# Performance work log

Hardware: AMD Instinct MI355X
Metric: run time of the kernel (lower is better)

Reference implementation:

```python
import jax, jax.numpy as jnp
import numpy as np

N_NODES = 100000
N_EDGES = 1600000
K = 3


def _cheb_conv(x, row, col, w, W, b):
    # SpMM: out[row] += w * x[col]
    def spmm(v):
        return jax.ops.segment_sum(w[:, None] * v[col], row, num_segments=N_NODES)
    Ts = [x, spmm(x)]
    for _ in range(2, K):
        Ts.append(2.0 * spmm(Ts[-1]) - Ts[-2])
    return jnp.concatenate(Ts, axis=-1) @ W.T + b


def setup_inputs() -> dict:
    key = jax.random.key(0)
    ks = jax.random.split(key, 12)
    inp = {
        "x": jax.random.normal(ks[0], (N_NODES, 128), dtype=jnp.float32),
        "edge_index": jax.random.randint(ks[1], (2, N_EDGES), 0, N_NODES, dtype=jnp.int32),
        "edge_weight": jax.random.normal(ks[2], (N_EDGES,), dtype=jnp.float32) * 0.05,
        "W_in": jax.random.normal(ks[3], (128, K * 128), dtype=jnp.float32) * (1.0 / np.sqrt(K * 128)),
        "b_in": jnp.zeros((128,), dtype=jnp.float32),
        "W_h1": jax.random.normal(ks[4], (128, K * 128), dtype=jnp.float32) * (1.0 / np.sqrt(K * 128)),
        "b_h1": jnp.zeros((128,), dtype=jnp.float32),
        "W_h2": jax.random.normal(ks[5], (128, K * 128), dtype=jnp.float32) * (1.0 / np.sqrt(K * 128)),
        "b_h2": jnp.zeros((128,), dtype=jnp.float32),
        "W_out": jax.random.normal(ks[6], (64, K * 128), dtype=jnp.float32) * (1.0 / np.sqrt(K * 128)),
        "b_out": jnp.zeros((64,), dtype=jnp.float32),
    }
    return inp


def reference(x, edge_index, edge_weight, W_in, b_in, W_h1, b_h1, W_h2, b_h2, W_out, b_out):
    row, col = edge_index[0], edge_index[1]
    # dropout is inactive at inference (training=False)
    h = jax.nn.relu(_cheb_conv(x, row, col, edge_weight, W_in, b_in))
    for (W, b) in ((W_h1, b_h1), (W_h2, b_h2)):
        h = jax.nn.relu(_cheb_conv(h, row, col, edge_weight, W, b) + h)  # residual
    out = _cheb_conv(h, row, col, edge_weight, W_out, b_out)
    return out
```

## Files before the change

### kernel.cpp

```cpp
#include <hip/hip_runtime.h>
#include <hip/hip_bf16.h>
#include <stdint.h>
#include <stddef.h>

#define N_NODES 100000
#define N_EDGES 1600000
#define FEAT 128
#define NB_SCAN ((N_NODES + 255) / 256)
#define LDS_PITCH 136
#define CAP 24
#define NL (CAP / 4)
#define NBKT ((N_NODES + 255) / 256)
#define BCAP 8160
#define EPB 2048

typedef __attribute__((ext_vector_type(8))) short bf16x8;
typedef __attribute__((ext_vector_type(4))) float f32x4;
typedef unsigned short u16;

__device__ __forceinline__ float bf2f(u16 u) {
    union { unsigned int i; float f; } v; v.i = ((unsigned int)u) << 16; return v.f;
}
__device__ __forceinline__ u16 f2bf(float f) {
    union { float f; unsigned int i; } v; v.f = f;
    unsigned int x = v.i;
    return (u16)((x + 0x7fffu + ((x >> 16) & 1u)) >> 16);
}


__global__ void hist_kernel(const int* __restrict__ rows, int* __restrict__ counts) {
    int e = blockIdx.x * blockDim.x + threadIdx.x;
    if (e < N_EDGES) {
        int r = rows[e];
        r = min(max(r, 0), N_NODES - 1);
        atomicAdd(&counts[r], 1);
    }
}

__global__ void reduce_counts_kernel(const int* __restrict__ counts, int* __restrict__ bsum) {
    __shared__ int s[256];
    int i = blockIdx.x * 256 + threadIdx.x;
    int v = (i < N_NODES) ? counts[i] : 0;
    s[threadIdx.x] = v; __syncthreads();
    for (int off = 128; off > 0; off >>= 1) {
        if (threadIdx.x < off) s[threadIdx.x] += s[threadIdx.x + off];
        __syncthreads();
    }
    if (threadIdx.x == 0) bsum[blockIdx.x] = s[0];
}

__global__ void scan_bsums_kernel(int* __restrict__ bsum, int* __restrict__ row_ptr) {
    __shared__ int s[512];
    int t = threadIdx.x;
    int v = (t < NB_SCAN) ? bsum[t] : 0;
    s[t] = v; __syncthreads();
    for (int off = 1; off < 512; off <<= 1) {
        int x = (t >= off) ? s[t - off] : 0;
        __syncthreads();
        s[t] += x;
        __syncthreads();
    }
    if (t < NB_SCAN) bsum[t] = s[t] - v;
    if (t == NB_SCAN - 1) row_ptr[N_NODES] = s[t];
}

__global__ void write_rowptr_kernel(int* __restrict__ counts, const int* __restrict__ bsum,
                                    int* __restrict__ row_ptr) {
    __shared__ int s[256];
    int i = blockIdx.x * 256 + threadIdx.x;
    int v = (i < N_NODES) ? counts[i] : 0;
    s[threadIdx.x] = v; __syncthreads();
    for (int off = 1; off < 256; off <<= 1) {
        int x = (threadIdx.x >= off) ? s[threadIdx.x - off] : 0;
        __syncthreads();
        s[threadIdx.x] += x;
        __syncthreads();
    }
    if (i < N_NODES) {
        row_ptr[i] = bsum[blockIdx.x] + s[threadIdx.x] - v;
        counts[i] = 0;
    }
}

__global__ void scatter_kernel(const int* __restrict__ rows, const int* __restrict__ cols,
                               const float* __restrict__ w, const int* __restrict__ row_ptr,
                               int* __restrict__ fill, int2* __restrict__ ecw) {
    int e = blockIdx.x * blockDim.x + threadIdx.x;
    if (e < N_EDGES) {
        int r = rows[e];
        r = min(max(r, 0), N_NODES - 1);
        int pos = row_ptr[r] + atomicAdd(&fill[r], 1);
        pos = min(max(pos, 0), N_EDGES - 1);
        int c = cols[e];
        c = min(max(c, 0), N_NODES - 1);
        ecw[pos] = make_int2(c, __float_as_int(w[e]));
    }
}


__global__ __launch_bounds__(256) void bucket_p1_kernel(const int* __restrict__ rows,
                                                        const int* __restrict__ cols,
                                                        const float* __restrict__ w,
                                                        int* __restrict__ gcnt,
                                                        int2* __restrict__ bbuf) {
    __shared__ int s_cnt[NBKT];
    __shared__ int s_base[NBKT];
    int tid = threadIdx.x;
    for (int b = tid; b < NBKT; b += 256) s_cnt[b] = 0;
    __syncthreads();
    int e0 = blockIdx.x * EPB;
#pragma unroll
    for (int it = 0; it < EPB / 256; ++it) {
        int e = e0 + it * 256 + tid;
        if (e < N_EDGES) {
            int r = min(max(rows[e], 0), N_NODES - 1);
            atomicAdd(&s_cnt[r >> 8], 1);
        }
    }
    __syncthreads();
    for (int b = tid; b < NBKT; b += 256) {
        s_base[b] = atomicAdd(&gcnt[b], s_cnt[b]);
        s_cnt[b] = 0;
    }
    __syncthreads();
#pragma unroll
    for (int it = 0; it < EPB / 256; ++it) {
        int e = e0 + it * 256 + tid;
        if (e < N_EDGES) {
            int r = min(max(rows[e], 0), N_NODES - 1);
            int b = r >> 8;
            int k = atomicAdd(&s_cnt[b], 1);
            int pos = min(s_base[b] + k, BCAP - 1);
            int c = min(max(cols[e], 0), N_NODES - 1);
            bbuf[(size_t)b * BCAP + pos] = make_int2(c | ((r & 255) << 20), __float_as_int(w[e]));
        }
    }
}

__global__ void scan_gcnt_kernel(const int* __restrict__ gcnt, int* __restrict__ bsum,
                                 int* __restrict__ row_ptr) {
    __shared__ int s[512];
    int t = threadIdx.x;
    int v = (t < NBKT) ? min(gcnt[t], BCAP) : 0;
    s[t] = v; __syncthreads();
    for (int off = 1; off < 512; off <<= 1) {
        int x = (t >= off) ? s[t - off] : 0;
        __syncthreads();
        s[t] += x;
        __syncthreads();
    }
    if (t < NBKT) bsum[t] = s[t] - v;
    if (t == NBKT - 1) row_ptr[N_NODES] = s[t];
}

__global__ __launch_bounds__(256) void bucket_finalize_kernel(const int* __restrict__ gcnt,
                                                              const int* __restrict__ bsum,
                                                              const int2* __restrict__ bbuf,
                                                              int* __restrict__ row_ptr,
                                                              int2* __restrict__ ecw) {
    __shared__ int s_cnt[256];
    __shared__ int s_pos[256];
    int b = blockIdx.x, tid = threadIdx.x;
    int base = bsum[b];
    int cnt = min(gcnt[b], BCAP);
    s_cnt[tid] = 0; __syncthreads();
    for (int i = tid; i < cnt; i += 256)
        atomicAdd(&s_cnt[bbuf[(size_t)b * BCAP + i].x >> 20], 1);
    __syncthreads();
    int v = s_cnt[tid];
    s_pos[tid] = v; __syncthreads();
    for (int off = 1; off < 256; off <<= 1) {
        int x = (tid >= off) ? s_pos[tid - off] : 0;
        __syncthreads();
        s_pos[tid] += x;
        __syncthreads();
    }
    int excl = s_pos[tid] - v;
    int r = b * 256 + tid;
    if (r < N_NODES) row_ptr[r] = base + excl;
    s_cnt[tid] = excl;
    __syncthreads();
    for (int i = tid; i < cnt; i += 256) {
        int2 p = bbuf[(size_t)b * BCAP + i];
        int rl = p.x >> 20;
        int pos = base + atomicAdd(&s_cnt[rl], 1);
        pos = min(max(pos, 0), N_EDGES - 1);
        ecw[pos] = make_int2(p.x & 0xFFFFF, p.y);
    }
}

__device__ __forceinline__ float w_fold(const float* W, int o, int k) {
    if (k < 128)      return W[o * 384 + k] - W[o * 384 + 256 + k];
    else if (k < 256) return W[o * 384 + k];
    else              return 2.0f * W[o * 384 + k];
}

__global__ void prep_w_kernel(const float* __restrict__ W, u16* __restrict__ Wp, int O) {
    int i = blockIdx.x * blockDim.x + threadIdx.x;
    if (i >= O * 384) return;
    int o = i / 384, k = i % 384;
    Wp[i] = f2bf(w_fold(W, o, k));
}

__global__ void prep_w2_all_kernel(const float* __restrict__ Wa, const float* __restrict__ Wb,
                                   const float* __restrict__ Wc, const float* __restrict__ Wd,
                                   u16* __restrict__ Pa, u16* __restrict__ Pb,
                                   u16* __restrict__ Pc, u16* __restrict__ Pd) {
    int i = blockIdx.x * blockDim.x + threadIdx.x;
    const float* W; u16* P; int il;
    if (i < 6144)       { W = Wa; P = Pa; il = i; }
    else if (i < 12288) { W = Wb; P = Pb; il = i - 6144; }
    else if (i < 18432) { W = Wc; P = Pc; il = i - 12288; }
    else if (i < 21504) { W = Wd; P = Pd; il = i - 18432; }
    else return;
    int ot = il / 768;
    int rem = il % 768;
    int kk = rem / 64;
    int l = rem % 64;
    int q = l >> 4, r = l & 15;
    int o = ot * 16 + r;
    int kbase = kk * 32 + q * 8;
#pragma unroll
    for (int j = 0; j < 8; ++j)
        P[(size_t)il * 8 + j] = f2bf(w_fold(W, o, kbase + j));
}


__global__ void cvt_kernel(const float* __restrict__ x, u16* __restrict__ y) {
    int i = blockIdx.x * blockDim.x + threadIdx.x;
    if (i >= N_NODES * FEAT / 4) return;
    float4 v = ((const float4*)x)[i];
    ushort4 o;
    o.x = f2bf(v.x); o.y = f2bf(v.y); o.z = f2bf(v.z); o.w = f2bf(v.w);
    ((ushort4*)y)[i] = o;
}


__device__ __forceinline__ void load_meta(const int2* __restrict__ ecw, int s, int n,
                                          int lane, int& call, float& wall) {
    int idx = s + max(0, min(lane, n - 1));
    idx = min(idx, N_EDGES - 1);
    int2 cw = ecw[idx];
    call = cw.x;
    wall = (lane < n) ? __int_as_float(cw.y) : 0.f;
}

__device__ __forceinline__ void issue_row(const u16* __restrict__ X, int call,
                                          int g, int f, bf16x8* q) {
#pragma unroll
    for (int k = 0; k < NL; ++k) {
        int col = __shfl(call, k * 4 + g);
        q[k] = *(const bf16x8*)(X + (size_t)col * FEAT + f * 8);
    }
}

__device__ __forceinline__ void reduce_row(const bf16x8* q, float wall,
                                           int g, float* acc) {
#pragma unroll
    for (int k = 0; k < NL; ++k) {
        float wj = __shfl(wall, k * 4 + g);
#pragma unroll
        for (int j = 0; j < 8; ++j) acc[j] += wj * bf2f((u16)q[k][j]);
    }
}


__global__ __launch_bounds__(256) void spmm1_kernel(const int* __restrict__ row_ptr,
                                                    const int2* __restrict__ ecw,
                                                    const u16* __restrict__ X,
                                                    u16* __restrict__ Y) {
    int lane = threadIdx.x & 63;
    int g = lane >> 4, f = lane & 15;
    int rr = (blockIdx.x * blockDim.x + threadIdx.x) >> 6;

    int s = row_ptr[rr], e = row_ptr[rr + 1];
    float acc[8];
#pragma unroll
    for (int j = 0; j < 8; ++j) acc[j] = 0.f;

    {
        int call; float wall;
        load_meta(ecw, s, min(e - s, CAP), lane, call, wall);
        bf16x8 q[NL];
        issue_row(X, call, g, f, q);
        reduce_row(q, wall, g, acc);
    }
    for (int cs = s + CAP; cs < e; cs += CAP) {
        int c2; float w2;
        load_meta(ecw, cs, min(e - cs, CAP), lane, c2, w2);
        bf16x8 qt[NL];
        issue_row(X, c2, g, f, qt);
        reduce_row(qt, w2, g, acc);
    }

#pragma unroll
    for (int j = 0; j < 8; ++j) {
        acc[j] += __shfl_xor(acc[j], 16);
        acc[j] += __shfl_xor(acc[j], 32);
    }
    if (g == 0) {
        u16 tmp[8];
#pragma unroll
        for (int j = 0; j < 8; ++j) tmp[j] = f2bf(acc[j]);
        *(bf16x8*)(Y + (size_t)rr * FEAT + f * 8) = *(const bf16x8*)tmp;
    }
}


__device__ __forceinline__ void gather4(const int* __restrict__ row_ptr,
                                        const int2* __restrict__ ecw,
                                        const u16* __restrict__ X,
                                        int r0, int lane, int g, int f,
                                        float acc[4][8]) {
    int s[4], e[4];
    int call[4]; float wall[4];
#pragma unroll
    for (int y = 0; y < 4; ++y) {
        s[y] = row_ptr[r0 + y];
        e[y] = row_ptr[r0 + y + 1];
    }
#pragma unroll
    for (int y = 0; y < 4; ++y)
        load_meta(ecw, s[y], min(e[y] - s[y], CAP), lane, call[y], wall[y]);
#pragma unroll
    for (int y = 0; y < 4; ++y)
#pragma unroll
        for (int j = 0; j < 8; ++j) acc[y][j] = 0.f;

    bf16x8 q0[NL], q1[NL], q2[NL], q3[NL];
    issue_row(X, call[0], g, f, q0);
    issue_row(X, call[1], g, f, q1);
    reduce_row(q0, wall[0], g, acc[0]);
    issue_row(X, call[2], g, f, q2);
    reduce_row(q1, wall[1], g, acc[1]);
    issue_row(X, call[3], g, f, q3);
    reduce_row(q2, wall[2], g, acc[2]);
    reduce_row(q3, wall[3], g, acc[3]);

#pragma unroll
    for (int y = 0; y < 4; ++y) {
        for (int cs = s[y] + CAP; cs < e[y]; cs += CAP) {
            int c2; float w2;
            load_meta(ecw, cs, min(e[y] - cs, CAP), lane, c2, w2);
            bf16x8 qt[NL];
            issue_row(X, c2, g, f, qt);
            reduce_row(qt, w2, g, acc[y]);
        }
    }

#pragma unroll
    for (int y = 0; y < 4; ++y)
#pragma unroll
        for (int j = 0; j < 8; ++j) {
            acc[y][j] += __shfl_xor(acc[y][j], 16);
            acc[y][j] += __shfl_xor(acc[y][j], 32);
        }
}

__global__ __launch_bounds__(256) void spmm_kernel(const int* __restrict__ row_ptr,
                                                   const int2* __restrict__ ecw,
                                                   const u16* __restrict__ X,
                                                   u16* __restrict__ Y) {
    int wid = threadIdx.x >> 6;
    int lane = threadIdx.x & 63;
    int g = lane >> 4, f = lane & 15;
    int r0 = blockIdx.x * 16 + wid * 4;

    float acc[4][8];
    gather4(row_ptr, ecw, X, r0, lane, g, f, acc);

    if (g == 0) {
#pragma unroll
        for (int y = 0; y < 4; ++y) {
            u16 tmp[8];
#pragma unroll
            for (int j = 0; j < 8; ++j) tmp[j] = f2bf(acc[y][j]);
            *(bf16x8*)(Y + (size_t)(r0 + y) * FEAT + f * 8) = *(const bf16x8*)tmp;
        }
    }
}


template <int O, bool RELU, bool RES, bool OUT_F32>
__global__ __launch_bounds__(256) void gemm_kernel(const u16* __restrict__ H,
                                                   const u16* __restrict__ T1,
                                                   const u16* __restrict__ S2,
                                                   const u16* __restrict__ Wp2,
                                                   const float* __restrict__ bias,
                                                   void* __restrict__ outv) {
    __shared__ __align__(16) u16 sA[3][32][LDS_PITCH];
    int tid = threadIdx.x;
    int m0 = blockIdx.x * 32;

#pragma unroll
    for (int p = 0; p < 3; ++p) {
        const u16* sp = (p == 0) ? H : (p == 1) ? T1 : S2;
#pragma unroll
        for (int u = 0; u < 2; ++u) {
            int unit = u * 256 + tid;
            int row = unit >> 4, seg = unit & 15;
            *(bf16x8*)&sA[p][row][seg * 8] =
                *(const bf16x8*)(sp + (size_t)(m0 + row) * FEAT + seg * 8);
        }
    }
    __syncthreads();

    int lane = tid & 63, wid = tid >> 6;
    int r = lane & 15, q = lane >> 4;
    constexpr int NW = O / 64;
    f32x4 acc0[NW], acc1[NW];
#pragma unroll
    for (int t = 0; t < NW; ++t) {
        acc0[t] = (f32x4){0.f, 0.f, 0.f, 0.f};
        acc1[t] = (f32x4){0.f, 0.f, 0.f, 0.f};
    }

#pragma unroll
    for (int kk = 0; kk < 12; ++kk) {
        int p = kk >> 2, ko = kk & 3;
        bf16x8 af0 = *(const bf16x8*)&sA[p][r][ko * 32 + q * 8];
        bf16x8 af1 = *(const bf16x8*)&sA[p][16 + r][ko * 32 + q * 8];
#pragma unroll
        for (int t = 0; t < NW; ++t) {
            int ot = wid * NW + t;
            bf16x8 bfr = *(const bf16x8*)(Wp2 + ((size_t)(ot * 12 + kk) * 64 + lane) * 8);
            acc0[t] = __builtin_amdgcn_mfma_f32_16x16x32_bf16(af0, bfr, acc0[t], 0, 0, 0);
            acc1[t] = __builtin_amdgcn_mfma_f32_16x16x32_bf16(af1, bfr, acc1[t], 0, 0, 0);
        }
    }

#pragma unroll
    for (int t = 0; t < NW; ++t) {
        int col = (wid * NW + t) * 16 + r;
        float bv = bias[col];
#pragma unroll
        for (int i = 0; i < 4; ++i) {
            int lrow = q * 4 + i;
            float v0 = acc0[t][i] + bv;
            if (RES)  v0 += bf2f(sA[0][lrow][col]);
            if (RELU) v0 = fmaxf(v0, 0.f);
            float v1 = acc1[t][i] + bv;
            if (RES)  v1 += bf2f(sA[0][16 + lrow][col]);
            if (RELU) v1 = fmaxf(v1, 0.f);
            if (OUT_F32) {
                ((float*)outv)[(size_t)(m0 + lrow) * O + col] = v0;
                ((float*)outv)[(size_t)(m0 + 16 + lrow) * O + col] = v1;
            } else {
                ((u16*)outv)[(size_t)(m0 + lrow) * O + col] = f2bf(v0);
                ((u16*)outv)[(size_t)(m0 + 16 + lrow) * O + col] = f2bf(v1);
            }
        }
    }
}


template <int O, bool RELU, bool RES, bool OUT_F32>
__global__ __launch_bounds__(256) void fused_gemm_kernel(const int* __restrict__ row_ptr,
                                                         const int2* __restrict__ ecw,
                                                         const u16* __restrict__ H,
                                                         const u16* __restrict__ T1,
                                                         const u16* __restrict__ Wp,
                                                         const float* __restrict__ bias,
                                                         void* __restrict__ outv) {
    __shared__ __align__(16) u16 sT[16 * LDS_PITCH];
    int wid = threadIdx.x >> 6;
    int lane = threadIdx.x & 63;
    int g = lane >> 4, f = lane & 15;
    int m0 = blockIdx.x * 16;

    {
        float acc[4][8];
        gather4(row_ptr, ecw, T1, m0 + wid * 4, lane, g, f, acc);
        if (g == 0) {
#pragma unroll
            for (int y = 0; y < 4; ++y) {
                u16 tmp[8];
#pragma unroll
                for (int j = 0; j < 8; ++j) tmp[j] = f2bf(acc[y][j]);
                *(bf16x8*)(sT + (wid * 4 + y) * LDS_PITCH + f * 8) = *(const bf16x8*)tmp;
            }
        }
    }
    __syncthreads();

    int r = f, q = g;
    constexpr int NT = O / 16;
    constexpr int NW = NT / 4;
    f32x4 acc[NW];
#pragma unroll
    for (int t = 0; t < NW; ++t) acc[t] = (f32x4){0.f, 0.f, 0.f, 0.f};

#pragma unroll
    for (int kk = 0; kk < 12; ++kk) {
        bf16x8 af;
        if (kk < 4)
            af = *(const bf16x8*)(H + (size_t)(m0 + r) * FEAT + kk * 32 + q * 8);
        else if (kk < 8)
            af = *(const bf16x8*)(T1 + (size_t)(m0 + r) * FEAT + (kk - 4) * 32 + q * 8);
        else
            af = *(const bf16x8*)(sT + r * LDS_PITCH + (kk - 8) * 32 + q * 8);
#pragma unroll
        for (int t = 0; t < NW; ++t) {
            int ot = wid * NW + t;
            bf16x8 bfr = *(const bf16x8*)(Wp + (size_t)(ot * 16 + r) * 384 + kk * 32 + q * 8);
            acc[t] = __builtin_amdgcn_mfma_f32_16x16x32_bf16(af, bfr, acc[t], 0, 0, 0);
        }
    }

#pragma unroll
    for (int t = 0; t < NW; ++t) {
        int col = (wid * NW + t) * 16 + r;
        float bv = bias[col];
#pragma unroll
        for (int i = 0; i < 4; ++i) {
            int row = m0 + q * 4 + i;
            float v = acc[t][i] + bv;
            if (RES)  v += bf2f(H[(size_t)row * FEAT + col]);
            if (RELU) v = fmaxf(v, 0.f);
            if (OUT_F32) ((float*)outv)[(size_t)row * O + col] = v;
            else         ((u16*)outv)[(size_t)row * O + col] = f2bf(v);
        }
    }
}


static inline size_t align_up(size_t x) { return (x + 255) & ~(size_t)255; }

extern "C" void kernel_launch(void* const* d_in, const int* in_sizes, int n_in,
                              void* d_out, int out_size, void* d_ws, size_t ws_size,
                              hipStream_t stream) {
    const float* x     = (const float*)d_in[0];
    const int*   ei    = (const int*)d_in[1];
    const float* ew    = (const float*)d_in[2];
    const float* W_in  = (const float*)d_in[3];
    const float* b_in  = (const float*)d_in[4];
    const float* W_h1  = (const float*)d_in[5];
    const float* b_h1  = (const float*)d_in[6];
    const float* W_h2  = (const float*)d_in[7];
    const float* b_h2  = (const float*)d_in[8];
    const float* W_out = (const float*)d_in[9];
    const float* b_out = (const float*)d_in[10];

    const int* rows = ei;
    const int* cols = ei + N_EDGES;

    char* w = (char*)d_ws;
    size_t off = 0;
    int* counts = (int*)(w + off);            off = align_up(off + (size_t)N_NODES * 4);
    int* row_ptr= (int*)(w + off);            off = align_up(off + (size_t)(N_NODES + 1) * 4);
    int* bsum   = (int*)(w + off);            off = align_up(off + 512 * 4);
    int2* ecw   = (int2*)(w + off);           off = align_up(off + (size_t)N_EDGES * 8);
    u16* t1     = (u16*)(w + off);            off = align_up(off + (size_t)N_NODES * FEAT * 2);
    u16* h      = (u16*)(w + off);            off = align_up(off + (size_t)N_NODES * FEAT * 2);
    u16* Wp_in  = (u16*)(w + off);            off = align_up(off + (size_t)128 * 384 * 2);
    u16* Wp_h1  = (u16*)(w + off);            off = align_up(off + (size_t)128 * 384 * 2);
    u16* Wp_h2  = (u16*)(w + off);            off = align_up(off + (size_t)128 * 384 * 2);
    u16* Wp_out = (u16*)(w + off);            off = align_up(off + (size_t)64 * 384 * 2);
    u16* s2     = (u16*)(w + off);            size_t off2 = align_up(off + (size_t)N_NODES * FEAT * 2);
    u16* W2_in  = (u16*)(w + off2);           off2 = align_up(off2 + (size_t)128 * 384 * 2);
    u16* W2_h1  = (u16*)(w + off2);           off2 = align_up(off2 + (size_t)128 * 384 * 2);
    u16* W2_h2  = (u16*)(w + off2);           off2 = align_up(off2 + (size_t)128 * 384 * 2);
    u16* W2_out = (u16*)(w + off2);           off2 = align_up(off2 + (size_t)64 * 384 * 2);
    int* gcnt   = (int*)(w + off2);           off2 = align_up(off2 + (size_t)NBKT * 4);
    const bool use_split = (ws_size >= off2);
    static_assert((size_t)NBKT * BCAP * 8 <= (size_t)N_NODES * FEAT * 2, "bucket buffer exceeds s2");

    cvt_kernel<<<(N_NODES * FEAT / 4 + 255) / 256, 256, 0, stream>>>(x, h);

    const int grid16 = N_NODES / 16;
    const int grid32 = N_NODES / 32;
    const int grid1  = N_NODES * 64 / 256;

    if (use_split) {
        hipMemsetAsync(gcnt, 0, (size_t)NBKT * 4, stream);
        int2* bbuf = (int2*)s2;
        bucket_p1_kernel<<<(N_EDGES + EPB - 1) / EPB, 256, 0, stream>>>(rows, cols, ew, gcnt, bbuf);
        scan_gcnt_kernel<<<1, 512, 0, stream>>>(gcnt, bsum, row_ptr);
        bucket_finalize_kernel<<<NBKT, 256, 0, stream>>>(gcnt, bsum, bbuf, row_ptr, ecw);

        prep_w2_all_kernel<<<(21504 + 255) / 256, 256, 0, stream>>>(
            W_in, W_h1, W_h2, W_out, W2_in, W2_h1, W2_h2, W2_out);

        spmm1_kernel<<<grid1, 256, 0, stream>>>(row_ptr, ecw, h, t1);
        spmm1_kernel<<<grid1, 256, 0, stream>>>(row_ptr, ecw, t1, s2);
        gemm_kernel<128, true, false, false><<<grid32, 256, 0, stream>>>(h, t1, s2, W2_in, b_in, h);
        spmm1_kernel<<<grid1, 256, 0, stream>>>(row_ptr, ecw, h, t1);
        spmm1_kernel<<<grid1, 256, 0, stream>>>(row_ptr, ecw, t1, s2);
        gemm_kernel<128, true, true, false><<<grid32, 256, 0, stream>>>(h, t1, s2, W2_h1, b_h1, h);
        spmm1_kernel<<<grid1, 256, 0, stream>>>(row_ptr, ecw, h, t1);
        spmm1_kernel<<<grid1, 256, 0, stream>>>(row_ptr, ecw, t1, s2);
        gemm_kernel<128, true, true, false><<<grid32, 256, 0, stream>>>(h, t1, s2, W2_h2, b_h2, h);
        spmm1_kernel<<<grid1, 256, 0, stream>>>(row_ptr, ecw, h, t1);
        spmm1_kernel<<<grid1, 256, 0, stream>>>(row_ptr, ecw, t1, s2);
        gemm_kernel<64, false, false, true><<<grid32, 256, 0, stream>>>(h, t1, s2, W2_out, b_out, d_out);
    } else {
        hipMemsetAsync(counts, 0, (size_t)N_NODES * 4, stream);
        hist_kernel<<<N_EDGES / 256, 256, 0, stream>>>(rows, counts);
        reduce_counts_kernel<<<NB_SCAN, 256, 0, stream>>>(counts, bsum);
        scan_bsums_kernel<<<1, 512, 0, stream>>>(bsum, row_ptr);
        write_rowptr_kernel<<<NB_SCAN, 256, 0, stream>>>(counts, bsum, row_ptr);
        scatter_kernel<<<N_EDGES / 256, 256, 0, stream>>>(rows, cols, ew, row_ptr, counts, ecw);

        prep_w_kernel<<<(128 * 384 + 255) / 256, 256, 0, stream>>>(W_in, Wp_in, 128);
        prep_w_kernel<<<(128 * 384 + 255) / 256, 256, 0, stream>>>(W_h1, Wp_h1, 128);
        prep_w_kernel<<<(128 * 384 + 255) / 256, 256, 0, stream>>>(W_h2, Wp_h2, 128);
        prep_w_kernel<<<(64 * 384 + 255) / 256, 256, 0, stream>>>(W_out, Wp_out, 64);

        spmm_kernel<<<grid16, 256, 0, stream>>>(row_ptr, ecw, h, t1);
        fused_gemm_kernel<128, true, false, false><<<grid16, 256, 0, stream>>>(
            row_ptr, ecw, h, t1, Wp_in, b_in, h);
        spmm_kernel<<<grid16, 256, 0, stream>>>(row_ptr, ecw, h, t1);
        fused_gemm_kernel<128, true, true, false><<<grid16, 256, 0, stream>>>(
            row_ptr, ecw, h, t1, Wp_h1, b_h1, h);
        spmm_kernel<<<grid16, 256, 0, stream>>>(row_ptr, ecw, h, t1);
        fused_gemm_kernel<128, true, true, false><<<grid16, 256, 0, stream>>>(
            row_ptr, ecw, h, t1, Wp_h2, b_h2, h);
        spmm_kernel<<<grid16, 256, 0, stream>>>(row_ptr, ecw, h, t1);
        fused_gemm_kernel<64, false, false, true><<<grid16, 256, 0, stream>>>(
            row_ptr, ecw, h, t1, Wp_out, b_out, d_out);
    }
}
```

Before: 726.1 us.

## Replace atomic bucket scatter with deterministic two-pass counting sort for CSR build

The CSR build now writes per-block bucket counts, scans them per bucket across blocks, and then scatters edges to exact offsets. Each block first sorts its edges by bucket in LDS so the global writes are grouped into contiguous runs. This removes the global atomics and the fixed per-bucket capacity BCAP with its clamping, which also makes the edge order deterministic. In exchange it adds two kernel launches, a per-block count array, a strided column scan, and extra LDS use in pass B.

```diff
diff --git a/kernel.cpp b/kernel.cpp
--- a/kernel.cpp
+++ b/kernel.cpp
@@ -11,8 +11,9 @@
 #define CAP 24
 #define NL (CAP / 4)
 #define NBKT ((N_NODES + 255) / 256)
-#define BCAP 8160
 #define EPB 2048
+#define NBLK ((N_EDGES + EPB - 1) / EPB)
+#define EPT (EPB / 256)
 
 typedef __attribute__((ext_vector_type(8))) short bf16x8;
 typedef __attribute__((ext_vector_type(4))) float f32x4;
@@ -98,19 +99,15 @@
 }
 
 
-__global__ __launch_bounds__(256) void bucket_p1_kernel(const int* __restrict__ rows,
-                                                        const int* __restrict__ cols,
-                                                        const float* __restrict__ w,
-                                                        int* __restrict__ gcnt,
-                                                        int2* __restrict__ bbuf) {
+__global__ __launch_bounds__(256) void csr_passA_kernel(const int* __restrict__ rows,
+                                                        int* __restrict__ pcnt) {
     __shared__ int s_cnt[NBKT];
-    __shared__ int s_base[NBKT];
-    int tid = threadIdx.x;
+    int tid = threadIdx.x, blk = blockIdx.x;
     for (int b = tid; b < NBKT; b += 256) s_cnt[b] = 0;
     __syncthreads();
-    int e0 = blockIdx.x * EPB;
-#pragma unroll
-    for (int it = 0; it < EPB / 256; ++it) {
+    int e0 = blk * EPB;
+#pragma unroll
+    for (int it = 0; it < EPT; ++it) {
         int e = e0 + it * 256 + tid;
         if (e < N_EDGES) {
             int r = min(max(rows[e], 0), N_NODES - 1);
@@ -118,54 +115,129 @@
         }
     }
     __syncthreads();
+    for (int b = tid; b < NBKT; b += 256)
+        pcnt[(size_t)blk * NBKT + b] = s_cnt[b];
+}
+
+__global__ __launch_bounds__(256) void csr_scanP_kernel(int* __restrict__ pcnt,
+                                                        int* __restrict__ gtot) {
+    __shared__ int s[256];
+    int b = blockIdx.x, tid = threadIdx.x;
+    int carry = 0;
+    for (int c = 0; c < (NBLK + 255) / 256; ++c) {
+        int idx = c * 256 + tid;
+        int v = (idx < NBLK) ? pcnt[(size_t)idx * NBKT + b] : 0;
+        s[tid] = v; __syncthreads();
+        for (int off = 1; off < 256; off <<= 1) {
+            int x = (tid >= off) ? s[tid - off] : 0;
+            __syncthreads();
+            s[tid] += x;
+            __syncthreads();
+        }
+        if (idx < NBLK) pcnt[(size_t)idx * NBKT + b] = carry + s[tid] - v;
+        carry += s[255];
+        __syncthreads();
+    }
+    if (tid == 0) gtot[b] = carry;
+}
+
+__global__ void csr_scanG_kernel(const int* __restrict__ gtot, int* __restrict__ bsum,
+                                 int* __restrict__ row_ptr) {
+    __shared__ int s[512];
+    int t = threadIdx.x;
+    int v = (t < NBKT) ? gtot[t] : 0;
+    s[t] = v; __syncthreads();
+    for (int off = 1; off < 512; off <<= 1) {
+        int x = (t >= off) ? s[t - off] : 0;
+        __syncthreads();
+        s[t] += x;
+        __syncthreads();
+    }
+    if (t < NBKT) bsum[t] = s[t] - v;
+    if (t == NBKT - 1) {
+        bsum[NBKT] = s[t];
+        row_ptr[N_NODES] = s[t];
+    }
+}
+
+__global__ __launch_bounds__(256) void csr_passB_kernel(const int* __restrict__ rows,
+                                                        const int* __restrict__ cols,
+                                                        const float* __restrict__ w,
+                                                        const int* __restrict__ pcnt,
+                                                        const int* __restrict__ bsum,
+                                                        int2* __restrict__ ebuf) {
+    __shared__ int s_base[NBKT];
+    __shared__ int s_cnt[NBKT];
+    __shared__ int s_off[NBKT];
+    __shared__ int s_scan[512];
+    __shared__ int2 s_sorted[EPB];
+    __shared__ int s_dst[EPB];
+    int tid = threadIdx.x, blk = blockIdx.x;
     for (int b = tid; b < NBKT; b += 256) {
-        s_base[b] = atomicAdd(&gcnt[b], s_cnt[b]);
+        s_base[b] = bsum[b] + pcnt[(size_t)blk * NBKT + b];
         s_cnt[b] = 0;
     }
     __syncthreads();
-#pragma unroll
-    for (int it = 0; it < EPB / 256; ++it) {
+    int e0 = blk * EPB;
+    int n = min(N_EDGES - e0, EPB);
+
+    int2 pay[EPT]; int pb[EPT];
+#pragma unroll
+    for (int it = 0; it < EPT; ++it) {
         int e = e0 + it * 256 + tid;
         if (e < N_EDGES) {
             int r = min(max(rows[e], 0), N_NODES - 1);
-            int b = r >> 8;
-            int k = atomicAdd(&s_cnt[b], 1);
-            int pos = min(s_base[b] + k, BCAP - 1);
             int c = min(max(cols[e], 0), N_NODES - 1);
-            bbuf[(size_t)b * BCAP + pos] = make_int2(c | ((r & 255) << 20), __float_as_int(w[e]));
-        }
-    }
-}
-
-__global__ void scan_gcnt_kernel(const int* __restrict__ gcnt, int* __restrict__ bsum,
-                                 int* __restrict__ row_ptr) {
-    __shared__ int s[512];
-    int t = threadIdx.x;
-    int v = (t < NBKT) ? min(gcnt[t], BCAP) : 0;
-    s[t] = v; __syncthreads();
+            pay[it] = make_int2(c | ((r & 255) << 20), __float_as_int(w[e]));
+            pb[it] = r >> 8;
+            atomicAdd(&s_cnt[pb[it]], 1);
+        } else {
+            pb[it] = -1;
+        }
+    }
+    __syncthreads();
+    s_scan[tid] = (tid < NBKT) ? s_cnt[tid] : 0;
+    s_scan[tid + 256] = (tid + 256 < NBKT) ? s_cnt[tid + 256] : 0;
+    __syncthreads();
     for (int off = 1; off < 512; off <<= 1) {
-        int x = (t >= off) ? s[t - off] : 0;
-        __syncthreads();
-        s[t] += x;
-        __syncthreads();
-    }
-    if (t < NBKT) bsum[t] = s[t] - v;
-    if (t == NBKT - 1) row_ptr[N_NODES] = s[t];
-}
-
-__global__ __launch_bounds__(256) void bucket_finalize_kernel(const int* __restrict__ gcnt,
-                                                              const int* __restrict__ bsum,
-                                                              const int2* __restrict__ bbuf,
-                                                              int* __restrict__ row_ptr,
-                                                              int2* __restrict__ ecw) {
+        int a = (tid >= off) ? s_scan[tid - off] : 0;
+        int b2 = (tid + 256 >= off) ? s_scan[tid + 256 - off] : 0;
+        __syncthreads();
+        s_scan[tid] += a;
+        s_scan[tid + 256] += b2;
+        __syncthreads();
+    }
+    for (int b = tid; b < NBKT; b += 256) {
+        s_off[b] = s_scan[b] - s_cnt[b];
+        s_cnt[b] = 0;
+    }
+    __syncthreads();
+#pragma unroll
+    for (int it = 0; it < EPT; ++it) {
+        if (pb[it] >= 0) {
+            int k = atomicAdd(&s_cnt[pb[it]], 1);
+            int slot = s_off[pb[it]] + k;
+            s_sorted[slot] = pay[it];
+            s_dst[slot] = s_base[pb[it]] + k;
+        }
+    }
+    __syncthreads();
+    for (int p = tid; p < n; p += 256)
+        ebuf[s_dst[p]] = s_sorted[p];
+}
+
+__global__ __launch_bounds__(256) void csr_finalize_kernel(const int* __restrict__ bsum,
+                                                           const int2* __restrict__ ebuf,
+                                                           int* __restrict__ row_ptr,
+                                                           int2* __restrict__ ecw) {
     __shared__ int s_cnt[256];
     __shared__ int s_pos[256];
     int b = blockIdx.x, tid = threadIdx.x;
     int base = bsum[b];
-    int cnt = min(gcnt[b], BCAP);
+    int cnt = bsum[b + 1] - base;
     s_cnt[tid] = 0; __syncthreads();
     for (int i = tid; i < cnt; i += 256)
-        atomicAdd(&s_cnt[bbuf[(size_t)b * BCAP + i].x >> 20], 1);
+        atomicAdd(&s_cnt[ebuf[base + i].x >> 20], 1);
     __syncthreads();
     int v = s_cnt[tid];
     s_pos[tid] = v; __syncthreads();
@@ -181,7 +253,7 @@
     s_cnt[tid] = excl;
     __syncthreads();
     for (int i = tid; i < cnt; i += 256) {
-        int2 p = bbuf[(size_t)b * BCAP + i];
+        int2 p = ebuf[base + i];
         int rl = p.x >> 20;
         int pos = base + atomicAdd(&s_cnt[rl], 1);
         pos = min(max(pos, 0), N_EDGES - 1);
@@ -561,9 +633,10 @@
     u16* W2_h1  = (u16*)(w + off2);           off2 = align_up(off2 + (size_t)128 * 384 * 2);
     u16* W2_h2  = (u16*)(w + off2);           off2 = align_up(off2 + (size_t)128 * 384 * 2);
     u16* W2_out = (u16*)(w + off2);           off2 = align_up(off2 + (size_t)64 * 384 * 2);
-    int* gcnt   = (int*)(w + off2);           off2 = align_up(off2 + (size_t)NBKT * 4);
+    int* pcnt   = (int*)(w + off2);           off2 = align_up(off2 + (size_t)NBLK * NBKT * 4);
+    int* gtot   = (int*)(w + off2);           off2 = align_up(off2 + (size_t)NBKT * 4);
     const bool use_split = (ws_size >= off2);
-    static_assert((size_t)NBKT * BCAP * 8 <= (size_t)N_NODES * FEAT * 2, "bucket buffer exceeds s2");
+    static_assert((size_t)N_EDGES * 8 <= (size_t)N_NODES * FEAT * 2, "ebuf exceeds s2");
 
     cvt_kernel<<<(N_NODES * FEAT / 4 + 255) / 256, 256, 0, stream>>>(x, h);
 
@@ -572,11 +645,12 @@
     const int grid1  = N_NODES * 64 / 256;
 
     if (use_split) {
-        hipMemsetAsync(gcnt, 0, (size_t)NBKT * 4, stream);
-        int2* bbuf = (int2*)s2;
-        bucket_p1_kernel<<<(N_EDGES + EPB - 1) / EPB, 256, 0, stream>>>(rows, cols, ew, gcnt, bbuf);
-        scan_gcnt_kernel<<<1, 512, 0, stream>>>(gcnt, bsum, row_ptr);
-        bucket_finalize_kernel<<<NBKT, 256, 0, stream>>>(gcnt, bsum, bbuf, row_ptr, ecw);
+        int2* ebuf = (int2*)s2;
+        csr_passA_kernel<<<NBLK, 256, 0, stream>>>(rows, pcnt);
+        csr_scanP_kernel<<<NBKT, 256, 0, stream>>>(pcnt, gtot);
+        csr_scanG_kernel<<<1, 512, 0, stream>>>(gtot, bsum, row_ptr);
+        csr_passB_kernel<<<NBLK, 256, 0, stream>>>(rows, cols, ew, pcnt, bsum, ebuf);
+        csr_finalize_kernel<<<NBKT, 256, 0, stream>>>(bsum, ebuf, row_ptr, ecw);
 
         prep_w2_all_kernel<<<(21504 + 255) / 256, 256, 0, stream>>>(
             W_in, W_h1, W_h2, W_out, W2_in, W2_h1, W2_h2, W2_out);
```

Measured after the change: 700.8 us. -3.5%, faster.
